# Kernel tuning notes

Hardware: AMD Instinct MI355X
Metric: run time of the kernel (lower is better)

## Reference

```python
import jax, jax.numpy as jnp
import numpy as np

N_WIRES = 8


def setup_inputs() -> dict:
    key = jax.random.key(0)
    k1, k2, k3 = jax.random.split(key, 3)
    B, S, E = 8, 1024, 64
    x = jax.random.normal(k1, (B, S, E), jnp.float32)
    theta = jax.random.normal(k2, (N_WIRES,), jnp.float32) * 0.1  # trainable RX angles (shared QLayer across heads)
    V_CAT = 16
    combine_w = jax.random.normal(k3, (E, V_CAT), jnp.float32) / jnp.sqrt(jnp.float32(V_CAT))
    combine_b = jnp.zeros((E,), jnp.float32)
    return {"x": x, "theta": theta, "combine_w": combine_w, "combine_b": combine_b}


def _cnot(state, c, t):
    # state: [N] + [2]*N_WIRES ; wire w lives on axis w+1
    ca, ta = c + 1, t + 1
    s0 = jax.lax.index_in_dim(state, 0, axis=ca, keepdims=False)
    s1 = jax.lax.index_in_dim(state, 1, axis=ca, keepdims=False)
    ta2 = ta - 1 if ta > ca else ta  # control axis was removed
    s1 = jnp.flip(s1, axis=ta2)      # flip target bit where control == 1
    return jnp.stack([s0, s1], axis=ca)


def _qlayer(angles, theta):
    # angles: [N, 8]. RX(x) then trainable RX(theta) on same wire == RX(x+theta).
    half = 0.5 * (angles + theta)
    amp0 = jnp.cos(half).astype(jnp.complex64)          # <0|RX|0>
    amp1 = (-1j) * jnp.sin(half).astype(jnp.complex64)  # <1|RX|0>
    N = angles.shape[0]
    # product state over 8 wires -> [N, 256]
    state = jnp.ones((N, 1), jnp.complex64)
    for w in range(N_WIRES):
        per = jnp.stack([amp0[:, w], amp1[:, w]], axis=-1)  # [N, 2]
        state = (state[:, :, None] * per[:, None, :]).reshape(N, -1)
    state = state.reshape((N,) + (2,) * N_WIRES)
    # CNOT chain 0->1, ..., 6->7, then ring closure 7->0
    for w in range(N_WIRES - 1):
        state = _cnot(state, w, w + 1)
    state = _cnot(state, N_WIRES - 1, 0)
    probs = state.real ** 2 + state.imag ** 2
    exps = []
    for w in range(N_WIRES):
        axes = tuple(ax for ax in range(1, N_WIRES + 1) if ax != w + 1)
        marg = probs.sum(axis=axes)  # [N, 2]
        exps.append(marg[:, 0] - marg[:, 1])  # <Z_w>
    return jnp.stack(exps, axis=-1)  # [N, 8]


def reference(x, theta, combine_w, combine_b):
    B, S, E = x.shape
    d_k = E // N_WIRES  # == 8 (encoder needs exactly 8 angles)
    heads = x.reshape(B, S, N_WIRES, d_k).transpose(0, 2, 1, 3)  # [B, H, S, 8]
    meas = _qlayer(heads.reshape(-1, d_k), theta).reshape(B, N_WIRES, S, N_WIRES)
    # torch.chunk(3, -1) on size 8 -> splits of 3, 3, 2
    q, k, v = meas[..., :3], meas[..., 3:6], meas[..., 6:]
    scores = jnp.einsum('bhsd,bhtd->bhst', q, k) / jnp.sqrt(jnp.float32(E))
    attn = jax.nn.softmax(scores, axis=-1)
    out = jnp.einsum('bhst,bhtd->bhsd', attn, v)          # [B, H, S, 2]
    out = out.transpose(0, 2, 1, 3).reshape(B, S, -1)     # [B, S, 16]
    return out @ combine_w.T + combine_b
```

## Files before the change

kernel.cpp:

```cpp
#include <hip/hip_runtime.h>

#define NB 8
#define NS 1024
#define NH 8
#define NMONO 56
#define NTREE 35


constexpr int PRED[NMONO] = {
    0,
    0, 0, 0,
    1, 2, 3, 2, 3, 3,
    4, 5, 6, 7, 8, 9, 7, 8, 9, 9,
    10,11,12,13,14,15,16,17,18,19,16,17,18,19,19,
    20,21,22,23,24,25,26,27,28,29,30,31,32,33,34,30,31,32,33,34,34};
constexpr int VARI[NMONO] = {
    0,
    0, 1, 2,
    0, 0, 0, 1, 1, 2,
    0, 0, 0, 0, 0, 0, 1, 1, 1, 2,
    0, 0, 0, 0, 0, 0, 0, 0, 0, 0, 1, 1, 1, 1, 2,
    0, 0, 0, 0, 0, 0, 0, 0, 0, 0, 0, 0, 0, 0, 0, 1, 1, 1, 1, 1, 2};
#define F6 0.166666666666667f
#define F12 0.0833333333333333f
#define F24 0.0416666666666667f
#define F120 0.00833333333333333f
constexpr float COEF[NMONO] = {
    1.f,
    1.f, 1.f, 1.f,
    0.5f, 1.f, 1.f, 0.5f, 1.f, 0.5f,
    F6, 0.5f, 0.5f, 0.5f, 1.f, 0.5f, F6, 0.5f, 0.5f, F6,
    F24, F6, F6, 0.25f, 0.5f, 0.25f, F6, 0.5f, 0.5f, F6, F24, F6, 0.25f, F6, F24,
    F120, F24, F24, F12, F6, F12, F12, 0.25f, 0.25f, F12, F24, F6, 0.25f, F6, F24,
    F120, F24, F12, F12, F24, F120};

__global__ __launch_bounds__(768) void fused_qattn_kernel(
        const float* __restrict__ x, const float* __restrict__ theta,
        const float* __restrict__ W, const float* __restrict__ bias,
        float* __restrict__ out) {
    __shared__ __align__(16) float redL[12][8][64];
    __shared__ __align__(16) float MhL[8 * 172];
    __shared__ float WtL[16 * 65];
    __shared__ float biasL[64];
    __shared__ float attL[32][17];

    const int tid = threadIdx.x;
    const int b = blockIdx.x >> 5;
    const int chunk = blockIdx.x & 31;
    const int s0 = chunk * 32;

    float th[8];
#pragma unroll
    for (int j = 0; j < 8; ++j) th[j] = theta[j];

    for (int i = tid; i < 1024; i += 768) WtL[(i & 15) * 65 + (i >> 4)] = W[i];
    if (tid < 64) biasL[tid] = bias[tid];

    const int chg = tid >> 8;
    const int tg  = tid & 255;
    const int h = tg & 7;
    const int tslot = tg >> 3;

    float acc[NMONO];
#pragma unroll
    for (int i = 0; i < NMONO; ++i) acc[i] = 0.f;

#pragma unroll 1
    for (int it = 0; it < 32; ++it) {
        const int t = tslot + 32 * it;
        const float4* xp = (const float4*)(x + ((size_t)(b * NS + t)) * 64 + h * 8);
        float4 lo = xp[0], hi = xp[1];
        float c0 = __cosf(lo.x + th[0]);
        float c1 = __cosf(lo.y + th[1]);
        float c2 = __cosf(lo.z + th[2]);
        float c3 = __cosf(lo.w + th[3]);
        float c4 = __cosf(hi.x + th[4]);
        float c5 = __cosf(hi.y + th[5]);
        float c6 = __cosf(hi.z + th[6]);
        float c7 = __cosf(hi.w + th[7]);
        float k0 = ((c0 * c1) * c2) * c3;
        float k1 = k0 * c4;
        float k2 = k1 * c5;
        float v0 = k2 * c6;
        float v1 = v0 * c7;
        float wch = (chg == 0) ? 1.f : ((chg == 1) ? v0 : v1);

        float mono[NTREE];
        mono[0] = wch;
        acc[0] += wch;
#pragma unroll
        for (int i = 1; i < NMONO; ++i) {
            float var = (VARI[i] == 0) ? k0 : ((VARI[i] == 1) ? k1 : k2);
            if (i < NTREE) {
                mono[i] = mono[PRED[i]] * var;
                acc[i] += mono[i];
            } else {
                acc[i] = fmaf(mono[PRED[i]], var, acc[i]);
            }
        }
    }

#pragma unroll
    for (int i = 0; i < NMONO; ++i) {
        float a = acc[i];
        a += __shfl_xor(a, 8); a += __shfl_xor(a, 16); a += __shfl_xor(a, 32);
        acc[i] = a;
    }

    const int wv = tid >> 6;
    const int l  = tid & 63;
    if (l < 8) {
        float* dst = &redL[wv][l][0];
#pragma unroll
        for (int g = 0; g < 14; ++g)
            ((float4*)dst)[g] = make_float4(acc[4*g], acc[4*g+1], acc[4*g+2], acc[4*g+3]);
    }
    __syncthreads();

    for (int e = tid; e < 8 * 168; e += 768) {
        const int hh = e / 168, j = e - hh * 168;
        const int c = j / 56, i = j - c * 56;
        float s = ((redL[c * 4 + 0][hh][i] + redL[c * 4 + 1][hh][i])
                 + (redL[c * 4 + 2][hh][i] + redL[c * 4 + 3][hh][i]));
        MhL[hh * 172 + j] = s * COEF[i];
    }
    __syncthreads();

    if (tid < 256) {
        const int eh = tid >> 5, sl = tid & 31;
        const int s = s0 + sl;
        const float4* xp = (const float4*)(x + ((size_t)(b * NS + s)) * 64 + eh * 8);
        float4 lo = xp[0], hi = xp[1];
        float c0 = __cosf(lo.x + th[0]);
        float c1 = __cosf(lo.y + th[1]);
        float c2 = __cosf(lo.z + th[2]);
        float c3 = __cosf(lo.w + th[3]);
        float c4 = __cosf(hi.x + th[4]);
        float c5 = __cosf(hi.y + th[5]);
        float c6 = __cosf(hi.z + th[6]);
        float c7 = __cosf(hi.w + th[7]);
        float m1 = c0 * c1;
        float m2 = m1 * c2;
        float m0 = ((c1 * c2) * (c3 * c4)) * ((c5 * c6) * c7);
        float q0 = m0 * 0.125f, q1 = m1 * 0.125f, q2 = m2 * 0.125f;

        float mono[NMONO];
        mono[0] = 1.f;
#pragma unroll
        for (int i = 1; i < NMONO; ++i)
            mono[i] = mono[PRED[i]] * ((VARI[i] == 0) ? q0 : ((VARI[i] == 1) ? q1 : q2));

        const float4* MS = (const float4*)&MhL[eh * 172];
        const float4* MA = (const float4*)&MhL[eh * 172 + 56];
        const float4* MB = (const float4*)&MhL[eh * 172 + 112];
        float aS = 0.f, aA = 0.f, aB = 0.f;
#pragma unroll
        for (int g = 0; g < 14; ++g) {
            float4 ms = MS[g], ma = MA[g], mb = MB[g];
            float p0 = mono[g * 4 + 0], p1 = mono[g * 4 + 1];
            float p2 = mono[g * 4 + 2], p3 = mono[g * 4 + 3];
            aS = fmaf(p0, ms.x, aS); aS = fmaf(p1, ms.y, aS);
            aS = fmaf(p2, ms.z, aS); aS = fmaf(p3, ms.w, aS);
            aA = fmaf(p0, ma.x, aA); aA = fmaf(p1, ma.y, aA);
            aA = fmaf(p2, ma.z, aA); aA = fmaf(p3, ma.w, aA);
            aB = fmaf(p0, mb.x, aB); aB = fmaf(p1, mb.y, aB);
            aB = fmaf(p2, mb.z, aB); aB = fmaf(p3, mb.w, aB);
        }
        float inv = 1.0f / aS;
        attL[sl][2 * eh]     = aA * inv;
        attL[sl][2 * eh + 1] = aB * inv;
    }
    __syncthreads();

    if (tid < 256) {
        const int e = tid & 63, r0 = tid >> 6;
#pragma unroll
        for (int j = 0; j < 8; ++j) {
            const int row = r0 + 4 * j;
            float acc2 = biasL[e];
#pragma unroll
            for (int jj = 0; jj < 16; ++jj)
                acc2 = fmaf(attL[row][jj], WtL[jj * 65 + e], acc2);
            out[((size_t)(b * NS + s0 + row)) * 64 + e] = acc2;
        }
    }
}

extern "C" void kernel_launch(void* const* d_in, const int* in_sizes, int n_in,
                              void* d_out, int out_size, void* d_ws, size_t ws_size,
                              hipStream_t stream) {
    const float* x     = (const float*)d_in[0];
    const float* theta = (const float*)d_in[1];
    const float* W     = (const float*)d_in[2];
    const float* bias  = (const float*)d_in[3];
    float* out = (float*)d_out;

    fused_qattn_kernel<<<dim3(NB * 32), dim3(768), 0, stream>>>(x, theta, W, bias, out);
}
```

Before: 85.52 us.

## Replace redundant per-block sequence reduction with partial sums and last-block finish

Previously every block looped over the whole sequence to build the per-batch moment sums, which repeated that reduction 32 times per batch. Now each block reduces only its own 32-token chunk and writes the partial moments to workspace. An atomic counter per batch elects the last-arriving block, which sums the 32 partials and computes all 1024 output rows for that batch. This trades the repeated work for a serialized tail in which only 8 blocks do the query and projection phase. It also relies on the workspace counters being in the expected state on every call, since nothing in this code resets them.

```diff
diff --git a/kernel.cpp b/kernel.cpp
--- a/kernel.cpp
+++ b/kernel.cpp
@@ -34,6 +34,185 @@
     F120, F24, F24, F12, F6, F12, F12, 0.25f, 0.25f, F12, F24, F6, 0.25f, F6, F24,
     F120, F24, F12, F12, F24, F120};
 
+#define PART_OFF 1024
+#define PART_STRIDE 1344
+#define WS_NEED ((size_t)(PART_OFF + 256 * PART_STRIDE) * 4)
+
+__global__ __launch_bounds__(768) void qattn_onepass(
+        const float* __restrict__ x, const float* __restrict__ theta,
+        const float* __restrict__ W, const float* __restrict__ bias,
+        float* __restrict__ out, float* __restrict__ ws) {
+    __shared__ __align__(16) float S[21376];
+    __shared__ unsigned lastFlag;
+
+    const int tid = threadIdx.x;
+    const int b = blockIdx.x >> 5;
+    const int chunk = blockIdx.x & 31;
+
+    if (blockIdx.y != 0) ((volatile float*)S)[20600 + tid] = theta[0];
+
+    float th[8];
+#pragma unroll
+    for (int j = 0; j < 8; ++j) th[j] = theta[j];
+
+    {
+        const int ch = tid >> 8;
+        const int tg = tid & 255;
+        const int h = tg & 7;
+        const int t5 = tg >> 3;
+        const int t = chunk * 32 + t5;
+
+        const float4* xp = (const float4*)(x + ((size_t)(b * NS + t)) * 64 + h * 8);
+        float4 lo = xp[0], hi = xp[1];
+        float c0 = __cosf(lo.x + th[0]);
+        float c1 = __cosf(lo.y + th[1]);
+        float c2 = __cosf(lo.z + th[2]);
+        float c3 = __cosf(lo.w + th[3]);
+        float c4 = __cosf(hi.x + th[4]);
+        float c5 = __cosf(hi.y + th[5]);
+        float c6 = __cosf(hi.z + th[6]);
+        float c7 = __cosf(hi.w + th[7]);
+        float k0 = ((c0 * c1) * c2) * c3;
+        float k1 = k0 * c4;
+        float k2 = k1 * c5;
+        float v0 = k2 * c6;
+        float v1 = v0 * c7;
+        float wch = (ch == 0) ? 1.f : ((ch == 1) ? v0 : v1);
+
+        float mono[NMONO];
+        mono[0] = wch;
+#pragma unroll
+        for (int i = 1; i < NMONO; ++i) {
+            float var = (VARI[i] == 0) ? k0 : ((VARI[i] == 1) ? k1 : k2);
+            mono[i] = mono[PRED[i]] * var;
+        }
+
+#pragma unroll
+        for (int i = 0; i < NMONO; ++i) {
+            float a = mono[i];
+            a += __shfl_xor(a, 8); a += __shfl_xor(a, 16); a += __shfl_xor(a, 32);
+            mono[i] = a;
+        }
+        const int wv = tid >> 6, l = tid & 63;
+        if (l < 8) {
+            float* dst = &S[wv * 512 + l * 64];
+#pragma unroll
+            for (int g = 0; g < 14; ++g)
+                ((float4*)dst)[g] = make_float4(mono[4*g], mono[4*g+1],
+                                                mono[4*g+2], mono[4*g+3]);
+        }
+    }
+    __syncthreads();
+
+    {
+        float* part = ws + PART_OFF + (size_t)blockIdx.x * PART_STRIDE;
+        for (int e = tid; e < 8 * 168; e += 768) {
+            const int hh = e / 168, j = e - hh * 168;
+            const int cc = j / 56, i = j - cc * 56;
+            float s = ((S[(cc*4+0)*512 + hh*64 + i] + S[(cc*4+1)*512 + hh*64 + i])
+                     + (S[(cc*4+2)*512 + hh*64 + i] + S[(cc*4+3)*512 + hh*64 + i]));
+            part[e] = s * COEF[i];
+        }
+    }
+
+    __threadfence();
+    __syncthreads();
+    if (tid == 0) {
+        unsigned P = ((volatile unsigned*)ws)[64];
+        unsigned old = atomicAdd((unsigned*)ws + b, 1u);
+        lastFlag = (old - P == 31u) ? 1u : 0u;
+    }
+    __syncthreads();
+    if (!lastFlag) return;
+    __threadfence();
+
+    {
+        const float* pbase = ws + PART_OFF + (size_t)(b * 32) * PART_STRIDE;
+        for (int e = tid; e < 8 * 168; e += 768) {
+            float s = 0.f;
+#pragma unroll
+            for (int c = 0; c < 32; ++c) s += pbase[c * PART_STRIDE + e];
+            const int hh = e / 168, j = e - hh * 168;
+            S[hh * 172 + j] = s;
+        }
+    }
+    for (int i = tid; i < 1024; i += 768) S[1376 + (i & 15) * 65 + (i >> 4)] = W[i];
+    if (tid < 64) S[2416 + tid] = bias[tid];
+    __syncthreads();
+
+    for (int half = 0; half < 2; ++half) {
+        for (int k = 0; k < 6; ++k) {
+            const int idx = tid + k * 768;
+            if (idx < 4096) {
+                const int eh = idx & 7, sl = idx >> 3;
+                const int s = half * 512 + sl;
+                const float4* xp = (const float4*)(x + ((size_t)(b * NS + s)) * 64 + eh * 8);
+                float4 lo = xp[0], hi = xp[1];
+                float c0 = __cosf(lo.x + th[0]);
+                float c1 = __cosf(lo.y + th[1]);
+                float c2 = __cosf(lo.z + th[2]);
+                float c3 = __cosf(lo.w + th[3]);
+                float c4 = __cosf(hi.x + th[4]);
+                float c5 = __cosf(hi.y + th[5]);
+                float c6 = __cosf(hi.z + th[6]);
+                float c7 = __cosf(hi.w + th[7]);
+                float m1 = c0 * c1;
+                float m2 = m1 * c2;
+                float m0 = ((c1 * c2) * (c3 * c4)) * ((c5 * c6) * c7);
+                float q0 = m0 * 0.125f, q1 = m1 * 0.125f, q2 = m2 * 0.125f;
+
+                float mono[NMONO];
+                mono[0] = 1.f;
+#pragma unroll
+                for (int i = 1; i < NMONO; ++i)
+                    mono[i] = mono[PRED[i]] * ((VARI[i] == 0) ? q0
+                                : ((VARI[i] == 1) ? q1 : q2));
+
+                const float4* MS = (const float4*)&S[eh * 172];
+                const float4* MA = (const float4*)&S[eh * 172 + 56];
+                const float4* MB = (const float4*)&S[eh * 172 + 112];
+                float aS = 0.f, aA = 0.f, aB = 0.f;
+#pragma unroll
+                for (int g = 0; g < 14; ++g) {
+                    float4 ms = MS[g], ma = MA[g], mb = MB[g];
+                    float p0 = mono[g*4+0], p1 = mono[g*4+1];
+                    float p2 = mono[g*4+2], p3 = mono[g*4+3];
+                    aS = fmaf(p0, ms.x, aS); aS = fmaf(p1, ms.y, aS);
+                    aS = fmaf(p2, ms.z, aS); aS = fmaf(p3, ms.w, aS);
+                    aA = fmaf(p0, ma.x, aA); aA = fmaf(p1, ma.y, aA);
+                    aA = fmaf(p2, ma.z, aA); aA = fmaf(p3, ma.w, aA);
+                    aB = fmaf(p0, mb.x, aB); aB = fmaf(p1, mb.y, aB);
+                    aB = fmaf(p2, mb.z, aB); aB = fmaf(p3, mb.w, aB);
+                }
+                float inv = 1.0f / aS;
+                S[2480 + sl * 17 + 2 * eh]     = aA * inv;
+                S[2480 + sl * 17 + 2 * eh + 1] = aB * inv;
+            }
+        }
+        __syncthreads();
+
+        for (int k = 0; k < 11; ++k) {
+            const int idx = tid + k * 768;
+            if (idx < 8192) {
+                const int e4 = idx & 15, sl = idx >> 4;
+                const int s = half * 512 + sl;
+                float a0 = S[2416 + e4*4 + 0], a1 = S[2416 + e4*4 + 1];
+                float a2 = S[2416 + e4*4 + 2], a3 = S[2416 + e4*4 + 3];
+#pragma unroll
+                for (int jj = 0; jj < 16; ++jj) {
+                    float av = S[2480 + sl * 17 + jj];
+                    const float* wr = &S[1376 + jj * 65 + e4 * 4];
+                    a0 = fmaf(av, wr[0], a0); a1 = fmaf(av, wr[1], a1);
+                    a2 = fmaf(av, wr[2], a2); a3 = fmaf(av, wr[3], a3);
+                }
+                *(float4*)(out + ((size_t)(b * NS + s)) * 64 + e4 * 4) =
+                    make_float4(a0, a1, a2, a3);
+            }
+        }
+        __syncthreads();
+    }
+}
+
 __global__ __launch_bounds__(768) void fused_qattn_kernel(
         const float* __restrict__ x, const float* __restrict__ theta,
         const float* __restrict__ W, const float* __restrict__ bias,
@@ -91,12 +270,8 @@
 #pragma unroll
         for (int i = 1; i < NMONO; ++i) {
             float var = (VARI[i] == 0) ? k0 : ((VARI[i] == 1) ? k1 : k2);
-            if (i < NTREE) {
-                mono[i] = mono[PRED[i]] * var;
-                acc[i] += mono[i];
-            } else {
-                acc[i] = fmaf(mono[PRED[i]], var, acc[i]);
-            }
+            if (i < NTREE) { mono[i] = mono[PRED[i]] * var; acc[i] += mono[i]; }
+            else           { acc[i] = fmaf(mono[PRED[i]], var, acc[i]); }
         }
     }
 
@@ -107,8 +282,7 @@
         acc[i] = a;
     }
 
-    const int wv = tid >> 6;
-    const int l  = tid & 63;
+    const int wv = tid >> 6, l = tid & 63;
     if (l < 8) {
         float* dst = &redL[wv][l][0];
 #pragma unroll
@@ -120,8 +294,8 @@
     for (int e = tid; e < 8 * 168; e += 768) {
         const int hh = e / 168, j = e - hh * 168;
         const int c = j / 56, i = j - c * 56;
-        float s = ((redL[c * 4 + 0][hh][i] + redL[c * 4 + 1][hh][i])
-                 + (redL[c * 4 + 2][hh][i] + redL[c * 4 + 3][hh][i]));
+        float s = ((redL[c*4+0][hh][i] + redL[c*4+1][hh][i])
+                 + (redL[c*4+2][hh][i] + redL[c*4+3][hh][i]));
         MhL[hh * 172 + j] = s * COEF[i];
     }
     __syncthreads();
@@ -157,8 +331,8 @@
 #pragma unroll
         for (int g = 0; g < 14; ++g) {
             float4 ms = MS[g], ma = MA[g], mb = MB[g];
-            float p0 = mono[g * 4 + 0], p1 = mono[g * 4 + 1];
-            float p2 = mono[g * 4 + 2], p3 = mono[g * 4 + 3];
+            float p0 = mono[g*4+0], p1 = mono[g*4+1];
+            float p2 = mono[g*4+2], p3 = mono[g*4+3];
             aS = fmaf(p0, ms.x, aS); aS = fmaf(p1, ms.y, aS);
             aS = fmaf(p2, ms.z, aS); aS = fmaf(p3, ms.w, aS);
             aA = fmaf(p0, ma.x, aA); aA = fmaf(p1, ma.y, aA);
@@ -195,5 +369,11 @@
     const float* bias  = (const float*)d_in[3];
     float* out = (float*)d_out;
 
-    fused_qattn_kernel<<<dim3(NB * 32), dim3(768), 0, stream>>>(x, theta, W, bias, out);
+    if (ws_size >= WS_NEED) {
+        qattn_onepass<<<dim3(NB * 32), dim3(768), 0, stream>>>(
+            x, theta, W, bias, out, (float*)d_ws);
+    } else {
+        fused_qattn_kernel<<<dim3(NB * 32), dim3(768), 0, stream>>>(
+            x, theta, W, bias, out);
+    }
 }
```

New measurement: 177.4 us. +107.4%, slower.

## Split into moments and evaluation kernels to stop recomputing moments per query chunk

Applied to the files above, without the earlier changes.

Adds a moments kernel that computes each head's polynomial moment sums once over key slices and writes partials to workspace. An evaluation kernel then sums the partials and does the per-query rational evaluation and output projection. This removes the redundant recomputation of full-sequence moments in every query-chunk block, at the cost of a second launch and a global round-trip. The old fused kernel is kept as a fallback when the workspace is too small.

```diff
diff --git a/kernel.cpp b/kernel.cpp
--- a/kernel.cpp
+++ b/kernel.cpp
@@ -34,6 +34,169 @@
     F120, F24, F24, F12, F6, F12, F12, 0.25f, 0.25f, F12, F24, F6, 0.25f, F6, F24,
     F120, F24, F12, F12, F24, F120};
 
+#define WS_NEED ((size_t)512 * 168 * sizeof(float))
+
+__global__ __launch_bounds__(192) void moments_kernel(
+        const float* __restrict__ x, const float* __restrict__ theta,
+        float* __restrict__ part) {
+    __shared__ float red[3][64][57];
+
+    const int tid = threadIdx.x;
+    const int bh = blockIdx.x >> 3;
+    const int qt = blockIdx.x & 7;
+    const int b = bh >> 3, h = bh & 7;
+    const int t0 = qt * 128;
+
+    float th[8];
+#pragma unroll
+    for (int j = 0; j < 8; ++j) th[j] = theta[j];
+
+    const int w = tid >> 6, l = tid & 63;
+
+    float acc[NMONO];
+#pragma unroll
+    for (int i = 0; i < NMONO; ++i) acc[i] = 0.f;
+
+#pragma unroll 1
+    for (int j = 0; j < 2; ++j) {
+        int t = t0 + l + 64 * j;
+        const float4* xp = (const float4*)(x + ((size_t)(b * NS + t)) * 64 + h * 8);
+        float4 lo = xp[0], hi = xp[1];
+        float c0 = __cosf(lo.x + th[0]);
+        float c1 = __cosf(lo.y + th[1]);
+        float c2 = __cosf(lo.z + th[2]);
+        float c3 = __cosf(lo.w + th[3]);
+        float c4 = __cosf(hi.x + th[4]);
+        float c5 = __cosf(hi.y + th[5]);
+        float c6 = __cosf(hi.z + th[6]);
+        float c7 = __cosf(hi.w + th[7]);
+        float k0 = ((c0 * c1) * c2) * c3;
+        float k1 = k0 * c4;
+        float k2 = k1 * c5;
+        float v0 = k2 * c6;
+        float v1 = v0 * c7;
+        float wch = (w == 0) ? 1.f : ((w == 1) ? v0 : v1);
+
+        float mono[NTREE];
+        mono[0] = wch;
+        acc[0] += wch;
+#pragma unroll
+        for (int i = 1; i < NMONO; ++i) {
+            float var = (VARI[i] == 0) ? k0 : ((VARI[i] == 1) ? k1 : k2);
+            if (i < NTREE) {
+                mono[i] = mono[PRED[i]] * var;
+                acc[i] += mono[i];
+            } else {
+                acc[i] = fmaf(mono[PRED[i]], var, acc[i]);
+            }
+        }
+    }
+#pragma unroll
+    for (int i = 0; i < NMONO; ++i) red[w][l][i] = acc[i];
+    __syncthreads();
+
+    if (l < NMONO) {
+        float s0 = 0.f, s1 = 0.f, s2 = 0.f, s3 = 0.f;
+#pragma unroll
+        for (int r = 0; r < 16; ++r) {
+            s0 += red[w][4 * r + 0][l];
+            s1 += red[w][4 * r + 1][l];
+            s2 += red[w][4 * r + 2][l];
+            s3 += red[w][4 * r + 3][l];
+        }
+        part[(size_t)blockIdx.x * 168 + w * 56 + l] = ((s0 + s1) + (s2 + s3)) * COEF[l];
+    }
+}
+
+__global__ __launch_bounds__(256) void eval_proj_kernel(
+        const float* __restrict__ x, const float* __restrict__ theta,
+        const float* __restrict__ part, const float* __restrict__ W,
+        const float* __restrict__ bias, float* __restrict__ out) {
+    __shared__ __align__(16) float MhL[8 * 172];
+    __shared__ float WtL[16 * 65];
+    __shared__ float biasL[64];
+    __shared__ float attL[32][17];
+
+    const int tid = threadIdx.x;
+    const int b = blockIdx.x >> 5;
+    const int chunk = blockIdx.x & 31;
+    const int s0 = chunk * 32;
+
+    float th[8];
+#pragma unroll
+    for (int j = 0; j < 8; ++j) th[j] = theta[j];
+
+    for (int e = tid; e < 8 * 168; e += 256) {
+        int h = e / 168, idx = e - h * 168;
+        const float* p = part + ((size_t)((b * 8 + h) * 8)) * 168 + idx;
+        float s = ((p[0] + p[168]) + (p[336] + p[504]))
+                + ((p[672] + p[840]) + (p[1008] + p[1176]));
+        MhL[h * 172 + idx] = s;
+    }
+    for (int i = tid; i < 1024; i += 256) WtL[(i & 15) * 65 + (i >> 4)] = W[i];
+    if (tid < 64) biasL[tid] = bias[tid];
+    __syncthreads();
+
+    {
+        const int eh = tid >> 5, sl = tid & 31;
+        const int s = s0 + sl;
+        const float4* xp = (const float4*)(x + ((size_t)(b * NS + s)) * 64 + eh * 8);
+        float4 lo = xp[0], hi = xp[1];
+        float c0 = __cosf(lo.x + th[0]);
+        float c1 = __cosf(lo.y + th[1]);
+        float c2 = __cosf(lo.z + th[2]);
+        float c3 = __cosf(lo.w + th[3]);
+        float c4 = __cosf(hi.x + th[4]);
+        float c5 = __cosf(hi.y + th[5]);
+        float c6 = __cosf(hi.z + th[6]);
+        float c7 = __cosf(hi.w + th[7]);
+        float m1 = c0 * c1;
+        float m2 = m1 * c2;
+        float m0 = ((c1 * c2) * (c3 * c4)) * ((c5 * c6) * c7);
+        float q0 = m0 * 0.125f, q1 = m1 * 0.125f, q2 = m2 * 0.125f;
+
+        float mono[NMONO];
+        mono[0] = 1.f;
+#pragma unroll
+        for (int i = 1; i < NMONO; ++i)
+            mono[i] = mono[PRED[i]] * ((VARI[i] == 0) ? q0 : ((VARI[i] == 1) ? q1 : q2));
+
+        const float4* MS = (const float4*)&MhL[eh * 172];
+        const float4* MA = (const float4*)&MhL[eh * 172 + 56];
+        const float4* MB = (const float4*)&MhL[eh * 172 + 112];
+        float aS = 0.f, aA = 0.f, aB = 0.f;
+#pragma unroll
+        for (int g = 0; g < 14; ++g) {
+            float4 ms = MS[g], ma = MA[g], mb = MB[g];
+            float p0 = mono[g * 4 + 0], p1 = mono[g * 4 + 1];
+            float p2 = mono[g * 4 + 2], p3 = mono[g * 4 + 3];
+            aS = fmaf(p0, ms.x, aS); aS = fmaf(p1, ms.y, aS);
+            aS = fmaf(p2, ms.z, aS); aS = fmaf(p3, ms.w, aS);
+            aA = fmaf(p0, ma.x, aA); aA = fmaf(p1, ma.y, aA);
+            aA = fmaf(p2, ma.z, aA); aA = fmaf(p3, ma.w, aA);
+            aB = fmaf(p0, mb.x, aB); aB = fmaf(p1, mb.y, aB);
+            aB = fmaf(p2, mb.z, aB); aB = fmaf(p3, mb.w, aB);
+        }
+        float inv = 1.0f / aS;
+        attL[sl][2 * eh]     = aA * inv;
+        attL[sl][2 * eh + 1] = aB * inv;
+    }
+    __syncthreads();
+
+    {
+        const int e = tid & 63, r0 = tid >> 6;
+#pragma unroll
+        for (int j = 0; j < 8; ++j) {
+            const int row = r0 + 4 * j;
+            float acc = biasL[e];
+#pragma unroll
+            for (int jj = 0; jj < 16; ++jj)
+                acc = fmaf(attL[row][jj], WtL[jj * 65 + e], acc);
+            out[((size_t)(b * NS + s0 + row)) * 64 + e] = acc;
+        }
+    }
+}
+
 __global__ __launch_bounds__(768) void fused_qattn_kernel(
         const float* __restrict__ x, const float* __restrict__ theta,
         const float* __restrict__ W, const float* __restrict__ bias,
@@ -91,12 +254,8 @@
 #pragma unroll
         for (int i = 1; i < NMONO; ++i) {
             float var = (VARI[i] == 0) ? k0 : ((VARI[i] == 1) ? k1 : k2);
-            if (i < NTREE) {
-                mono[i] = mono[PRED[i]] * var;
-                acc[i] += mono[i];
-            } else {
-                acc[i] = fmaf(mono[PRED[i]], var, acc[i]);
-            }
+            if (i < NTREE) { mono[i] = mono[PRED[i]] * var; acc[i] += mono[i]; }
+            else           { acc[i] = fmaf(mono[PRED[i]], var, acc[i]); }
         }
     }
 
@@ -107,8 +266,7 @@
         acc[i] = a;
     }
 
-    const int wv = tid >> 6;
-    const int l  = tid & 63;
+    const int wv = tid >> 6, l = tid & 63;
     if (l < 8) {
         float* dst = &redL[wv][l][0];
 #pragma unroll
@@ -120,8 +278,8 @@
     for (int e = tid; e < 8 * 168; e += 768) {
         const int hh = e / 168, j = e - hh * 168;
         const int c = j / 56, i = j - c * 56;
-        float s = ((redL[c * 4 + 0][hh][i] + redL[c * 4 + 1][hh][i])
-                 + (redL[c * 4 + 2][hh][i] + redL[c * 4 + 3][hh][i]));
+        float s = ((redL[c*4+0][hh][i] + redL[c*4+1][hh][i])
+                 + (redL[c*4+2][hh][i] + redL[c*4+3][hh][i]));
         MhL[hh * 172 + j] = s * COEF[i];
     }
     __syncthreads();
@@ -157,8 +315,8 @@
 #pragma unroll
         for (int g = 0; g < 14; ++g) {
             float4 ms = MS[g], ma = MA[g], mb = MB[g];
-            float p0 = mono[g * 4 + 0], p1 = mono[g * 4 + 1];
-            float p2 = mono[g * 4 + 2], p3 = mono[g * 4 + 3];
+            float p0 = mono[g*4+0], p1 = mono[g*4+1];
+            float p2 = mono[g*4+2], p3 = mono[g*4+3];
             aS = fmaf(p0, ms.x, aS); aS = fmaf(p1, ms.y, aS);
             aS = fmaf(p2, ms.z, aS); aS = fmaf(p3, ms.w, aS);
             aA = fmaf(p0, ma.x, aA); aA = fmaf(p1, ma.y, aA);
@@ -195,5 +353,11 @@
     const float* bias  = (const float*)d_in[3];
     float* out = (float*)d_out;
 
-    fused_qattn_kernel<<<dim3(NB * 32), dim3(768), 0, stream>>>(x, theta, W, bias, out);
+    if (ws_size >= WS_NEED) {
+        float* part = (float*)d_ws;
+        moments_kernel<<<dim3(512), dim3(192), 0, stream>>>(x, theta, part);
+        eval_proj_kernel<<<dim3(256), dim3(256), 0, stream>>>(x, theta, part, W, bias, out);
+    } else {
+        fused_qattn_kernel<<<dim3(NB * 32), dim3(768), 0, stream>>>(x, theta, W, bias, out);
+    }
 }
```

Result: faster. 68.86 us (-19.5%).
